# Kernel optimization log

Measured on AMD Instinct MI355X. Metric: run time of the kernel, lower is better.

The kernel has to match this reference:

```python
import jax, jax.numpy as jnp
import numpy as np

NUM_ROUTING = 3


def squash(s):
    # NOTE: original torch code sums the squared norm over axis=2 (the
    # out-capsule axis of s_j [B,1,O,Do]), NOT the feature axis. Faithful copy.
    norm = jnp.sum(s * s, axis=2, keepdims=True)
    scale = norm / (1.0 + norm) / jnp.sqrt(norm + 1e-9)
    return scale * s


def setup_inputs() -> dict:
    key = jax.random.key(0)
    k1, k2 = jax.random.split(key)
    B, N, Di, O, Do = 64, 8192, 8, 10, 16
    x = jax.random.normal(k1, (B, N, Di), dtype=jnp.float32)
    W = 0.01 * jax.random.normal(k2, (1, N, O, Do, Di), dtype=jnp.float32)
    return {"x": x, "W": W}


def reference(x, W):
    # x: [B, N, Di]; W: [1, N, O, Do, Di]
    N = x.shape[1]
    O = W.shape[2]
    # u_hat = W @ x per (n, o): [B, N, O, Do]
    u_hat = jnp.einsum('nodi,bni->bnod', W[0], x)
    b_ij = jnp.zeros((1, N, O, 1), dtype=x.dtype)
    v_j = None
    for r in range(NUM_ROUTING):
        c_ij = jax.nn.softmax(b_ij, axis=2)            # softmax over out caps
        s_j = jnp.sum(c_ij * u_hat, axis=1, keepdims=True)  # [B,1,O,Do]
        v_j = squash(s_j)
        if r < NUM_ROUTING - 1:
            # agreement: broadcasts b_ij to [B,N,O,1] after first update
            b_ij = b_ij + jnp.sum(u_hat * v_j, axis=-1, keepdims=True)
    return v_j[:, 0]  # [B, O, Do]
```

## Files before the change

### kernel.cpp

```cpp
#include <hip/hip_runtime.h>

typedef unsigned int u32;
typedef unsigned short u16;
typedef _Float16 h2 __attribute__((ext_vector_type(2)));
typedef _Float16 h4 __attribute__((ext_vector_type(4)));
typedef float f4 __attribute__((ext_vector_type(4)));

#define B_ 64
#define N_ 8192
#define DI 8
#define O_ 10
#define DO_ 16
#define OD 160
#define NCHUNK 32
#define NPART 256
#define CHN 4
#define NCHK (NCHUNK / CHN)
#define WROW (OD * DI)
#define CHH (CHN * WROW)
#define CSTR 164

static __device__ __forceinline__ h2 pkrtz(float a, float b) {
    return __builtin_bit_cast(h2, __builtin_amdgcn_cvt_pkrtz(a, b));
}

template <int PHASE, int TAIL>
__global__ __launch_bounds__(512, 2)
void caps_pass(const float* __restrict__ Xf, const float* __restrict__ Wf,
               const u16* __restrict__ Vb, float* __restrict__ Sout,
               _Float16* __restrict__ Sh) {
    __shared__ float smem[B_ * CSTR];
    _Float16* stage = (_Float16*)smem;

    const int tid  = threadIdx.x;
    const int lane = tid & 63;
    const int c    = lane & 15;
    const int hh   = lane >> 4;
    const int w    = __builtin_amdgcn_readfirstlane(tid >> 6);
    const int tau  = w & 3, eta = w >> 2;
    const int b    = tau * 16 + c;
    const int nb   = blockIdx.x * NCHUNK;

    const int a32  = (lane ^ 32) << 2;

    int off[5];
    #pragma unroll
    for (int k = 0; k < 5; ++k) off[k] = (tid + k * 512) * 2;

    float2 st[5];
    {
        const float* src = Wf + (size_t)nb * WROW;
        #pragma unroll
        for (int k = 0; k < 5; ++k) st[k] = *(const float2*)(src + off[k]);
        #pragma unroll
        for (int k = 0; k < 5; ++k)
            *(h2*)&stage[off[k]] = pkrtz(st[k].x, st[k].y);
    }

    f4 vv[O_];
    if (PHASE > 0) {
        const _Float16* vp = (const _Float16*)Vb + (size_t)b * OD + 4 * hh;
        #pragma unroll
        for (int oo = 0; oo < O_; ++oo) {
            const h4 hv = *(const h4*)(vp + oo * DO_);
            vv[oo][0] = (float)hv[0]; vv[oo][1] = (float)hv[1];
            vv[oo][2] = (float)hv[2]; vv[oo][3] = (float)hv[3];
        }
    }

    const f4 fz = {0.f, 0.f, 0.f, 0.f};
    f4 acc[O_];
    #pragma unroll
    for (int oo = 0; oo < O_; ++oo) acc[oo] = fz;

    const int ioff = (hh < 2) ? 4 * hh : 0;
    const float* xb = Xf + ((size_t)b * N_ + nb + eta * 2) * DI + ioff;
    float4 xcur = *(const float4*)xb;

    __syncthreads();

    #pragma unroll 1
    for (int ch = 0; ch < NCHK; ++ch) {
        if (ch < NCHK - 1) {
            const float* src = Wf + (size_t)(nb + (ch + 1) * CHN) * WROW;
            #pragma unroll
            for (int k = 0; k < 5; ++k) st[k] = *(const float2*)(src + off[k]);
        }
        const _Float16* wb = stage + (ch & 1) * CHH;

        #pragma unroll
        for (int kk = 0; kk < 2; ++kk) {
            const int s = ch * 2 + kk;
            float4 xnext = xcur;
            if (s < 15) {
                const int s1 = s + 1;
                xnext = *(const float4*)(xb + ((s1 >> 1) * CHN + (s1 & 1)) * DI);
            }

            h4 bf = {(_Float16)0.f, (_Float16)0.f, (_Float16)0.f, (_Float16)0.f};
            if (hh < 2) {
                const h2 lo = pkrtz(xcur.x, xcur.y);
                const h2 hi = pkrtz(xcur.z, xcur.w);
                bf[0] = lo[0]; bf[1] = lo[1]; bf[2] = hi[0]; bf[3] = hi[1];
            }
            xcur = xnext;

            const _Float16* wr = wb + (eta * 2 + kk) * WROW + c * DI + ioff;
            f4 u[O_];
            #pragma unroll
            for (int oo = 0; oo < O_; ++oo) {
                h4 af = {(_Float16)0.f, (_Float16)0.f, (_Float16)0.f, (_Float16)0.f};
                if (hh < 2) af = *(const h4*)(wr + oo * (DO_ * DI));
                if (PHASE == 0) {
                    acc[oo] = __builtin_amdgcn_mfma_f32_16x16x16f16(af, bf, acc[oo], 0, 0, 0);
                } else {
                    u[oo] = __builtin_amdgcn_mfma_f32_16x16x16f16(af, bf, fz, 0, 0, 0);
                }
            }

            if (PHASE > 0) {
                float tex[O_];
                #pragma unroll
                for (int q = 0; q < 5; ++q) {
                    const int o0 = 2 * q, o1 = 2 * q + 1;
                    const float p0 = u[o0][0]*vv[o0][0] + u[o0][1]*vv[o0][1]
                                   + u[o0][2]*vv[o0][2] + u[o0][3]*vv[o0][3];
                    const float p1 = u[o1][0]*vv[o1][0] + u[o1][1]*vv[o1][1]
                                   + u[o1][2]*vv[o1][2] + u[o1][3]*vv[o1][3];
                    h2 pk = pkrtz(p0, p1);
                    int pi = __builtin_bit_cast(int, pk);
                    pk = pk + __builtin_bit_cast(h2, __builtin_amdgcn_ds_swizzle(pi, 0x401F));
                    pi = __builtin_bit_cast(int, pk);
                    pk = pk + __builtin_bit_cast(h2, __builtin_amdgcn_ds_bpermute(a32, pi));
                    tex[o0] = __expf((float)pk[0]);
                    tex[o1] = __expf((float)pk[1]);
                }
                const float den = (((tex[0] + tex[1]) + (tex[2] + tex[3]))
                                 + ((tex[4] + tex[5]) + (tex[6] + tex[7])))
                                 + (tex[8] + tex[9]);
                const float rinv = 1.0f / den;
                #pragma unroll
                for (int oo = 0; oo < O_; ++oo) {
                    const float co = tex[oo] * rinv;
                    acc[oo][0] = fmaf(co, u[oo][0], acc[oo][0]);
                    acc[oo][1] = fmaf(co, u[oo][1], acc[oo][1]);
                    acc[oo][2] = fmaf(co, u[oo][2], acc[oo][2]);
                    acc[oo][3] = fmaf(co, u[oo][3], acc[oo][3]);
                }
            }
        }

        if (ch < NCHK - 1) {
            _Float16* dst = stage + ((ch + 1) & 1) * CHH;
            #pragma unroll
            for (int k = 0; k < 5; ++k)
                *(h2*)&dst[off[k]] = pkrtz(st[k].x, st[k].y);
        }
        __syncthreads();
    }

    if (eta == 1) {
        #pragma unroll
        for (int oo = 0; oo < O_; ++oo)
            *(f4*)&smem[b * CSTR + oo * DO_ + 4 * hh] = acc[oo];
    }
    __syncthreads();
    if (eta == 0) {
        #pragma unroll
        for (int oo = 0; oo < O_; ++oo)
            acc[oo] = acc[oo] + *(const f4*)&smem[b * CSTR + oo * DO_ + 4 * hh];
        const float sc = (PHASE == 0) ? 0.1f : 1.0f;
        if (TAIL == 1) {
            _Float16* my = Sh + (size_t)blockIdx.x * (B_ * OD) + (size_t)b * OD;
            #pragma unroll
            for (int oo = 0; oo < O_; ++oo) {
                h4 hq;
                hq[0] = (_Float16)(sc * acc[oo][0]);
                hq[1] = (_Float16)(sc * acc[oo][1]);
                hq[2] = (_Float16)(sc * acc[oo][2]);
                hq[3] = (_Float16)(sc * acc[oo][3]);
                *(h4*)(my + oo * DO_ + 4 * hh) = hq;
            }
        } else {
            float* Sg = Sout + (size_t)b * OD;
            #pragma unroll
            for (int oo = 0; oo < O_; ++oo) {
                atomicAdd(&Sg[oo * DO_ + 4 * hh + 0], sc * acc[oo][0]);
                atomicAdd(&Sg[oo * DO_ + 4 * hh + 1], sc * acc[oo][1]);
                atomicAdd(&Sg[oo * DO_ + 4 * hh + 2], sc * acc[oo][2]);
                atomicAdd(&Sg[oo * DO_ + 4 * hh + 3], sc * acc[oo][3]);
            }
        }
    }
}

template <int PHASE>
__global__ __launch_bounds__(1024)
void caps_reduce_fin(const _Float16* __restrict__ Sp, int nparts,
                     float* __restrict__ V0f, u16* __restrict__ Vb,
                     float* __restrict__ out) {
    __shared__ float sg[6 * OD];
    __shared__ float s_s[OD];
    __shared__ float s_scale[DO_];
    const int b = blockIdx.x;
    const int t = threadIdx.x;
    if (t < 6 * OD) {
        const int g = t / OD, od = t - g * OD;
        float acc = 0.0f;
        const _Float16* p0 = Sp + (size_t)b * OD + od;
        #pragma unroll 4
        for (int p = g; p < nparts; p += 6)
            acc += (float)p0[(size_t)p * (B_ * OD)];
        sg[t] = acc;
    }
    __syncthreads();
    if (t < OD) {
        float s = 0.0f;
        #pragma unroll
        for (int gg = 0; gg < 6; ++gg) s += sg[gg * OD + t];
        s_s[t] = s;
    }
    __syncthreads();
    if (t < DO_) {
        float norm = 0.0f;
        #pragma unroll
        for (int o = 0; o < O_; ++o) { float x = s_s[o * DO_ + t]; norm = fmaf(x, x, norm); }
        s_scale[t] = norm / (1.0f + norm) * rsqrtf(norm + 1e-9f);
    }
    __syncthreads();
    if (t < OD) {
        const float v = s_s[t] * s_scale[t & 15];
        const int idx = b * OD + t;
        if (PHASE == 0) {
            V0f[idx] = v;
            _Float16 h = (_Float16)v;
            Vb[idx] = __builtin_bit_cast(u16, h);
        } else if (PHASE == 1) {
            const float vs = V0f[idx] + v;
            _Float16 h = (_Float16)vs;
            Vb[idx] = __builtin_bit_cast(u16, h);
        } else {
            out[idx] = v;
        }
    }
}

template <int PHASE>
__global__ __launch_bounds__(1024)
void caps_finalize(float* __restrict__ S, float* __restrict__ V0f,
                   u16* __restrict__ Vb, float* __restrict__ out) {
    const int tid = threadIdx.x;
    const int b = tid >> 4, d = tid & 15;
    float sv[O_];
    float norm = 0.0f;
    #pragma unroll
    for (int o = 0; o < O_; ++o) {
        sv[o] = S[b * OD + o * DO_ + d];
        norm = fmaf(sv[o], sv[o], norm);
    }
    const float scale = norm / (1.0f + norm) * rsqrtf(norm + 1e-9f);
    #pragma unroll
    for (int o = 0; o < O_; ++o) {
        const int idx = b * OD + o * DO_ + d;
        const float v = scale * sv[o];
        if (PHASE == 0) {
            V0f[idx] = v;
            _Float16 hcv = (_Float16)v;
            Vb[idx] = __builtin_bit_cast(u16, hcv);
            S[idx] = 0.0f;
        } else if (PHASE == 1) {
            const float vs = V0f[idx] + v;
            _Float16 hcv = (_Float16)vs;
            Vb[idx] = __builtin_bit_cast(u16, hcv);
            S[idx] = 0.0f;
        } else {
            out[idx] = v;
        }
    }
}

extern "C" void kernel_launch(void* const* d_in, const int* in_sizes, int n_in,
                              void* d_out, int out_size, void* d_ws, size_t ws_size,
                              hipStream_t stream) {
    const float* Xf = (const float*)d_in[0];
    const float* Wf = (const float*)d_in[1];
    float* out = (float*)d_out;

    const size_t velems = (size_t)B_ * OD;
    const size_t base = velems * 4 + velems * 2;
    const size_t need = base + (size_t)NPART * velems * 2;

    float* V0f = (float*)d_ws;
    u16* Vb = (u16*)(V0f + velems);
    const dim3 grid(N_ / NCHUNK), blk(512), rgrid(B_), rblk(1024);

    if (ws_size >= need) {
        _Float16* P = (_Float16*)((char*)d_ws + base);
        caps_pass<0, 1><<<grid, blk, 0, stream>>>(Xf, Wf, nullptr, nullptr, P);
        caps_reduce_fin<0><<<rgrid, rblk, 0, stream>>>(P, NPART, V0f, Vb, nullptr);
        caps_pass<1, 1><<<grid, blk, 0, stream>>>(Xf, Wf, Vb, nullptr, P);
        caps_reduce_fin<1><<<rgrid, rblk, 0, stream>>>(P, NPART, V0f, Vb, nullptr);
        caps_pass<1, 1><<<grid, blk, 0, stream>>>(Xf, Wf, Vb, nullptr, P);
        caps_reduce_fin<2><<<rgrid, rblk, 0, stream>>>(P, NPART, nullptr, nullptr, out);
    } else {
        float* S = (float*)((char*)d_ws + base);
        const dim3 one(1), fblk(1024);
        (void)hipMemsetAsync(S, 0, velems * sizeof(float), stream);
        caps_pass<0, 2><<<grid, blk, 0, stream>>>(Xf, Wf, nullptr, S, nullptr);
        caps_finalize<0><<<one, fblk, 0, stream>>>(S, V0f, Vb, nullptr);
        caps_pass<1, 2><<<grid, blk, 0, stream>>>(Xf, Wf, Vb, S, nullptr);
        caps_finalize<1><<<one, fblk, 0, stream>>>(S, V0f, Vb, nullptr);
        caps_pass<1, 2><<<grid, blk, 0, stream>>>(Xf, Wf, Vb, S, nullptr);
        caps_finalize<2><<<one, fblk, 0, stream>>>(S, nullptr, nullptr, out);
    }
}
```

Before: 166.7 us.

## Shrink capsule-pass blocks to 256 threads with more, smaller N-chunks

The capsule pass now uses 256-thread blocks that each handle 8 input capsules instead of 32. This drops the two-wave split over N and its shared-memory cross-wave reduction, and the grid grows to 1024 blocks. The goal is to fill the GPU better and cut per-block shared memory and sync cost. The trade-off is four times as many fp16 partial sums, which the reduce kernel must read, and its unroll is raised to match.

```diff
diff --git a/kernel.cpp b/kernel.cpp
--- a/kernel.cpp
+++ b/kernel.cpp
@@ -12,32 +12,37 @@
 #define O_ 10
 #define DO_ 16
 #define OD 160
-#define NCHUNK 32
-#define NPART 256
-#define CHN 4
+#define NCHUNK 8
+#define NPART 1024
+#define CHN 2
 #define NCHK (NCHUNK / CHN)
 #define WROW (OD * DI)
 #define CHH (CHN * WROW)
-#define CSTR 164
 
 static __device__ __forceinline__ h2 pkrtz(float a, float b) {
     return __builtin_bit_cast(h2, __builtin_amdgcn_cvt_pkrtz(a, b));
 }
 
+static __device__ __forceinline__ h2 hsum4(h2 v, int a32) {
+    int pi = __builtin_bit_cast(int, v);
+    h2 pk = v + __builtin_bit_cast(h2, __builtin_amdgcn_ds_swizzle(pi, 0x401F));
+    pi = __builtin_bit_cast(int, pk);
+    pk = pk + __builtin_bit_cast(h2, __builtin_amdgcn_ds_bpermute(a32, pi));
+    return pk;
+}
+
 template <int PHASE, int TAIL>
-__global__ __launch_bounds__(512, 2)
+__global__ __launch_bounds__(256, 3)
 void caps_pass(const float* __restrict__ Xf, const float* __restrict__ Wf,
                const u16* __restrict__ Vb, float* __restrict__ Sout,
                _Float16* __restrict__ Sh) {
-    __shared__ float smem[B_ * CSTR];
-    _Float16* stage = (_Float16*)smem;
+    __shared__ _Float16 stage[2 * CHH];
 
     const int tid  = threadIdx.x;
     const int lane = tid & 63;
     const int c    = lane & 15;
     const int hh   = lane >> 4;
-    const int w    = __builtin_amdgcn_readfirstlane(tid >> 6);
-    const int tau  = w & 3, eta = w >> 2;
+    const int tau  = __builtin_amdgcn_readfirstlane(tid >> 6);
     const int b    = tau * 16 + c;
     const int nb   = blockIdx.x * NCHUNK;
 
@@ -45,7 +50,7 @@
 
     int off[5];
     #pragma unroll
-    for (int k = 0; k < 5; ++k) off[k] = (tid + k * 512) * 2;
+    for (int k = 0; k < 5; ++k) off[k] = (tid + k * 256) * 2;
 
     float2 st[5];
     {
@@ -74,7 +79,7 @@
     for (int oo = 0; oo < O_; ++oo) acc[oo] = fz;
 
     const int ioff = (hh < 2) ? 4 * hh : 0;
-    const float* xb = Xf + ((size_t)b * N_ + nb + eta * 2) * DI + ioff;
+    const float* xb = Xf + ((size_t)b * N_ + nb) * DI + ioff;
     float4 xcur = *(const float4*)xb;
 
     __syncthreads();
@@ -89,13 +94,11 @@
         const _Float16* wb = stage + (ch & 1) * CHH;
 
         #pragma unroll
-        for (int kk = 0; kk < 2; ++kk) {
-            const int s = ch * 2 + kk;
+        for (int kk = 0; kk < CHN; ++kk) {
+            const int s = ch * CHN + kk;
             float4 xnext = xcur;
-            if (s < 15) {
-                const int s1 = s + 1;
-                xnext = *(const float4*)(xb + ((s1 >> 1) * CHN + (s1 & 1)) * DI);
-            }
+            if (s < NCHUNK - 1)
+                xnext = *(const float4*)(xb + (size_t)(s + 1) * DI);
 
             h4 bf = {(_Float16)0.f, (_Float16)0.f, (_Float16)0.f, (_Float16)0.f};
             if (hh < 2) {
@@ -105,7 +108,7 @@
             }
             xcur = xnext;
 
-            const _Float16* wr = wb + (eta * 2 + kk) * WROW + c * DI + ioff;
+            const _Float16* wr = wb + kk * WROW + c * DI + ioff;
             f4 u[O_];
             #pragma unroll
             for (int oo = 0; oo < O_; ++oo) {
@@ -127,11 +130,7 @@
                                    + u[o0][2]*vv[o0][2] + u[o0][3]*vv[o0][3];
                     const float p1 = u[o1][0]*vv[o1][0] + u[o1][1]*vv[o1][1]
                                    + u[o1][2]*vv[o1][2] + u[o1][3]*vv[o1][3];
-                    h2 pk = pkrtz(p0, p1);
-                    int pi = __builtin_bit_cast(int, pk);
-                    pk = pk + __builtin_bit_cast(h2, __builtin_amdgcn_ds_swizzle(pi, 0x401F));
-                    pi = __builtin_bit_cast(int, pk);
-                    pk = pk + __builtin_bit_cast(h2, __builtin_amdgcn_ds_bpermute(a32, pi));
+                    const h2 pk = hsum4(pkrtz(p0, p1), a32);
                     tex[o0] = __expf((float)pk[0]);
                     tex[o1] = __expf((float)pk[1]);
                 }
@@ -159,37 +158,26 @@
         __syncthreads();
     }
 
-    if (eta == 1) {
-        #pragma unroll
-        for (int oo = 0; oo < O_; ++oo)
-            *(f4*)&smem[b * CSTR + oo * DO_ + 4 * hh] = acc[oo];
-    }
-    __syncthreads();
-    if (eta == 0) {
-        #pragma unroll
-        for (int oo = 0; oo < O_; ++oo)
-            acc[oo] = acc[oo] + *(const f4*)&smem[b * CSTR + oo * DO_ + 4 * hh];
-        const float sc = (PHASE == 0) ? 0.1f : 1.0f;
-        if (TAIL == 1) {
-            _Float16* my = Sh + (size_t)blockIdx.x * (B_ * OD) + (size_t)b * OD;
-            #pragma unroll
-            for (int oo = 0; oo < O_; ++oo) {
-                h4 hq;
-                hq[0] = (_Float16)(sc * acc[oo][0]);
-                hq[1] = (_Float16)(sc * acc[oo][1]);
-                hq[2] = (_Float16)(sc * acc[oo][2]);
-                hq[3] = (_Float16)(sc * acc[oo][3]);
-                *(h4*)(my + oo * DO_ + 4 * hh) = hq;
-            }
-        } else {
-            float* Sg = Sout + (size_t)b * OD;
-            #pragma unroll
-            for (int oo = 0; oo < O_; ++oo) {
-                atomicAdd(&Sg[oo * DO_ + 4 * hh + 0], sc * acc[oo][0]);
-                atomicAdd(&Sg[oo * DO_ + 4 * hh + 1], sc * acc[oo][1]);
-                atomicAdd(&Sg[oo * DO_ + 4 * hh + 2], sc * acc[oo][2]);
-                atomicAdd(&Sg[oo * DO_ + 4 * hh + 3], sc * acc[oo][3]);
-            }
+    const float sc = (PHASE == 0) ? 0.1f : 1.0f;
+    if (TAIL == 1) {
+        _Float16* my = Sh + (size_t)blockIdx.x * (B_ * OD) + (size_t)b * OD;
+        #pragma unroll
+        for (int oo = 0; oo < O_; ++oo) {
+            h4 hq;
+            hq[0] = (_Float16)(sc * acc[oo][0]);
+            hq[1] = (_Float16)(sc * acc[oo][1]);
+            hq[2] = (_Float16)(sc * acc[oo][2]);
+            hq[3] = (_Float16)(sc * acc[oo][3]);
+            *(h4*)(my + oo * DO_ + 4 * hh) = hq;
+        }
+    } else {
+        float* Sg = Sout + (size_t)b * OD;
+        #pragma unroll
+        for (int oo = 0; oo < O_; ++oo) {
+            atomicAdd(&Sg[oo * DO_ + 4 * hh + 0], sc * acc[oo][0]);
+            atomicAdd(&Sg[oo * DO_ + 4 * hh + 1], sc * acc[oo][1]);
+            atomicAdd(&Sg[oo * DO_ + 4 * hh + 2], sc * acc[oo][2]);
+            atomicAdd(&Sg[oo * DO_ + 4 * hh + 3], sc * acc[oo][3]);
         }
     }
 }
@@ -208,7 +196,7 @@
         const int g = t / OD, od = t - g * OD;
         float acc = 0.0f;
         const _Float16* p0 = Sp + (size_t)b * OD + od;
-        #pragma unroll 4
+        #pragma unroll 8
         for (int p = g; p < nparts; p += 6)
             acc += (float)p0[(size_t)p * (B_ * OD)];
         sg[t] = acc;
@@ -292,7 +280,7 @@
 
     float* V0f = (float*)d_ws;
     u16* Vb = (u16*)(V0f + velems);
-    const dim3 grid(N_ / NCHUNK), blk(512), rgrid(B_), rblk(1024);
+    const dim3 grid(N_ / NCHUNK), blk(256), rgrid(B_), rblk(1024);
 
     if (ws_size >= need) {
         _Float16* P = (_Float16*)((char*)d_ws + base);
```

New measurement: 281.0 us. +68.6%, slower.
